# Optimization experiments

Hardware: AMD Instinct MI355X
Metric: run time of the kernel (lower is better)

Reference implementation:

```python
import jax, jax.numpy as jnp
import numpy as np

T, B, V, E, H = 128, 32, 32000, 512, 1024
PAD = 0

def setup_inputs() -> dict:
    key = jax.random.key(0)
    ks = jax.random.split(key, 10)
    indices = jax.random.randint(ks[0], (T, B), 0, V)
    emb = jax.random.normal(ks[1], (V, E), jnp.float32) * 0.02
    s = 1.0 / np.sqrt(H).astype(np.float32)
    W_ih = jax.random.normal(ks[2], (4 * H, E), jnp.float32) * s
    W_hh = jax.random.normal(ks[3], (4 * H, H), jnp.float32) * s
    b_ih = jax.random.normal(ks[4], (4 * H,), jnp.float32) * 0.01
    b_hh = jax.random.normal(ks[5], (4 * H,), jnp.float32) * 0.01
    W_out = jax.random.normal(ks[6], (V, H), jnp.float32) * s
    b_out = jnp.zeros((V,), jnp.float32)
    h0 = jax.random.uniform(ks[7], (B, H), jnp.float32, -0.1, 0.1)
    c0 = jax.random.uniform(ks[8], (B, H), jnp.float32, -0.1, 0.1)
    return dict(indices=indices, emb=emb, W_ih=W_ih, W_hh=W_hh,
                b_ih=b_ih, b_hh=b_hh, W_out=W_out, b_out=b_out, h0=h0, c0=c0)

def reference(indices, emb, W_ih, W_hh, b_ih, b_hh, W_out, b_out, h0, c0):
    # embed + relu for all timesteps at once (dropout_rate=0.0 -> identity)
    x_all = jax.nn.relu(emb[indices[:-1]])   # [T-1, B, E]
    targets = indices[1:]                    # [T-1, B]

    def step(carry, inp):
        h, c, loss = carry
        x, tgt = inp
        # torch LSTM gate order: i, f, g, o
        gates = x @ W_ih.T + b_ih + h @ W_hh.T + b_hh   # [B, 4H]
        i, f, g, o = jnp.split(gates, 4, axis=-1)
        c = jax.nn.sigmoid(f) * c + jax.nn.sigmoid(i) * jnp.tanh(g)
        h = jax.nn.sigmoid(o) * jnp.tanh(c)
        logp = jax.nn.log_softmax(h @ W_out.T + b_out, axis=-1)  # [B, V]
        nll = -jnp.take_along_axis(logp, tgt[:, None], axis=-1)[:, 0]
        # NLLLoss(reduction='sum', ignore_index=PAD)
        loss = loss + jnp.sum(jnp.where(tgt != PAD, nll, 0.0))
        return (h, c, loss), None

    (_, _, loss), _ = jax.lax.scan(step, (h0, c0, jnp.float32(0.0)), (x_all, targets))
    return loss
```

## Files before the change

### kernel.cpp

```cpp
#include <hip/hip_runtime.h>
#include <hip/hip_bf16.h>
#include <hip/hip_cooperative_groups.h>
#include <math.h>

namespace cg = cooperative_groups;

typedef __bf16 bf16_t;
typedef bf16_t bf16x8 __attribute__((ext_vector_type(8)));
typedef float f32x4 __attribute__((ext_vector_type(4)));

#define T_SEQ 128
#define NB 32
#define NV 32000
#define NE 512
#define NH 1024
#define G4 4096
#define MROWS 4064
#define MPAD 4096

#define NBLK 256

__device__ __forceinline__ void g2lds16(const bf16_t* g, bf16_t* l) {
  __builtin_amdgcn_global_load_lds((const __attribute__((address_space(1))) void*)g,
                                   (__attribute__((address_space(3))) void*)l, 16, 0, 0);
}

__device__ __forceinline__ unsigned short bf16bits(float x) {
  bf16_t b = (bf16_t)x;
  return __builtin_bit_cast(unsigned short, b);
}

__global__ void k_prep(const int* __restrict__ idx, const float* __restrict__ emb,
                       const float* __restrict__ W_ih, const float* __restrict__ W_hh,
                       const float* __restrict__ b_ih, const float* __restrict__ b_hh,
                       const float* __restrict__ W_out, const float* __restrict__ h0,
                       bf16_t* __restrict__ W_ih_bf, bf16_t* __restrict__ W_hh_bf,
                       bf16_t* __restrict__ W_out_bf, bf16_t* __restrict__ x_bf,
                       bf16_t* __restrict__ h_all, bf16_t* __restrict__ h0_bf,
                       float* __restrict__ bc, float* __restrict__ rowS,
                       int* __restrict__ tgt, unsigned* __restrict__ bar) {
  const long nW_ih = 4096L * 512;
  const long nW_hh = 4096L * 1024;
  const long nW_out = 32000L * 1024;
  const long nX = 4096L * 512;
  const long nH0 = 32L * 1024;
  const long nHpad = 32L * 1024;
  const long NTOTAL = nW_ih + nW_hh + nW_out + nX + nH0 + nHpad + 3 * 4096L + 1024;
  long stride = (long)gridDim.x * blockDim.x;
  for (long i = (long)blockIdx.x * blockDim.x + threadIdx.x; i < NTOTAL; i += stride) {
    long j = i;
    if (j < nW_ih) { W_ih_bf[j] = (bf16_t)W_ih[j]; continue; }
    j -= nW_ih;
    if (j < nW_hh) { W_hh_bf[j] = (bf16_t)W_hh[j]; continue; }
    j -= nW_hh;
    if (j < nW_out) { W_out_bf[j] = (bf16_t)W_out[j]; continue; }
    j -= nW_out;
    if (j < nX) {
      long m = j >> 9; int e = (int)(j & 511);
      float x = 0.f;
      if (m < MROWS) { x = emb[(long)idx[m] * NE + e]; x = x > 0.f ? x : 0.f; }
      x_bf[j] = (bf16_t)x; continue;
    }
    j -= nX;
    if (j < nH0) { h0_bf[j] = (bf16_t)h0[j]; continue; }
    j -= nH0;
    if (j < nHpad) { h_all[4161536L + j] = (bf16_t)0.f; continue; }
    j -= nHpad;
    if (j < 4096) { bc[j] = b_ih[j] + b_hh[j]; continue; }
    j -= 4096;
    if (j < 4096) { rowS[j] = 0.f; continue; }
    j -= 4096;
    if (j < 4096) { tgt[j] = (j < MROWS) ? idx[j + NB] : 0; continue; }
    j -= 4096;
    { bar[j] = 0u; continue; }
  }
}

__global__ __launch_bounds__(256) void k_gemm1(const bf16_t* __restrict__ A,
                                               const bf16_t* __restrict__ B,
                                               const float* __restrict__ bc,
                                               bf16_t* __restrict__ C) {
  const int K = 512;
  int tid = threadIdx.x, wid = tid >> 6, lane = tid & 63;
  int wm = wid & 1, wn = wid >> 1;
  int quad = lane >> 4, l15 = lane & 15;
  int mBase = blockIdx.x * 64, nBase = blockIdx.y * 128;

  const bf16x8* pa0 = (const bf16x8*)(A + (long)(mBase + wm * 32 + l15) * K + quad * 8);
  const bf16x8* pa1 = (const bf16x8*)(A + (long)(mBase + wm * 32 + 16 + l15) * K + quad * 8);
  const bf16x8* pb[4];
#pragma unroll
  for (int j = 0; j < 4; ++j)
    pb[j] = (const bf16x8*)(B + (long)(nBase + wn * 64 + j * 16 + l15) * K + quad * 8);

  f32x4 acc[2][4];
#pragma unroll
  for (int mi = 0; mi < 2; ++mi)
#pragma unroll
    for (int ni = 0; ni < 4; ++ni) acc[mi][ni] = (f32x4){0.f, 0.f, 0.f, 0.f};

  for (int kk = 0; kk < K / 32; ++kk) {
    bf16x8 a0 = pa0[kk * 4], a1 = pa1[kk * 4];
    bf16x8 b0 = pb[0][kk * 4], b1 = pb[1][kk * 4], b2 = pb[2][kk * 4], b3 = pb[3][kk * 4];
    acc[0][0] = __builtin_amdgcn_mfma_f32_16x16x32_bf16(a0, b0, acc[0][0], 0, 0, 0);
    acc[0][1] = __builtin_amdgcn_mfma_f32_16x16x32_bf16(a0, b1, acc[0][1], 0, 0, 0);
    acc[0][2] = __builtin_amdgcn_mfma_f32_16x16x32_bf16(a0, b2, acc[0][2], 0, 0, 0);
    acc[0][3] = __builtin_amdgcn_mfma_f32_16x16x32_bf16(a0, b3, acc[0][3], 0, 0, 0);
    acc[1][0] = __builtin_amdgcn_mfma_f32_16x16x32_bf16(a1, b0, acc[1][0], 0, 0, 0);
    acc[1][1] = __builtin_amdgcn_mfma_f32_16x16x32_bf16(a1, b1, acc[1][1], 0, 0, 0);
    acc[1][2] = __builtin_amdgcn_mfma_f32_16x16x32_bf16(a1, b2, acc[1][2], 0, 0, 0);
    acc[1][3] = __builtin_amdgcn_mfma_f32_16x16x32_bf16(a1, b3, acc[1][3], 0, 0, 0);
  }
#pragma unroll
  for (int ni = 0; ni < 4; ++ni) {
    int col = nBase + wn * 64 + ni * 16 + l15;
    float bcv = bc[col];
#pragma unroll
    for (int mi = 0; mi < 2; ++mi)
#pragma unroll
      for (int r = 0; r < 4; ++r) {
        int row = mBase + wm * 32 + mi * 16 + quad * 4 + r;
        C[(long)row * G4 + col] = (bf16_t)(acc[mi][ni][r] + bcv);
      }
  }
}

__device__ __forceinline__ void lbar(unsigned* grp, unsigned* root, unsigned* gen,
                                     unsigned target) {
  __syncthreads();
  if (threadIdx.x == 0) {
    asm volatile("" ::: "memory");
    __builtin_amdgcn_s_waitcnt(0x0f70);
    unsigned o = __hip_atomic_fetch_add(grp, 1u, __ATOMIC_RELAXED,
                                        __HIP_MEMORY_SCOPE_AGENT);
    if ((o & 15u) == 15u) {
      unsigned r = __hip_atomic_fetch_add(root, 1u, __ATOMIC_RELAXED,
                                          __HIP_MEMORY_SCOPE_AGENT);
      if ((r & 7u) == 7u)
        __hip_atomic_store(gen, (r >> 3) + 1u, __ATOMIC_RELAXED,
                           __HIP_MEMORY_SCOPE_AGENT);
    }
    while (__hip_atomic_load(gen, __ATOMIC_RELAXED, __HIP_MEMORY_SCOPE_AGENT) < target)
      __builtin_amdgcn_s_sleep(1);
    asm volatile("" ::: "memory");
  }
  __syncthreads();
}

__global__ __launch_bounds__(512) void k_rec4(const bf16_t* __restrict__ gates_x,
                                              const bf16_t* __restrict__ W_hh_bf,
                                              const bf16_t* __restrict__ h0_bf,
                                              bf16_t* __restrict__ h_all,
                                              const float* __restrict__ c0,
                                              unsigned* __restrict__ bar) {
  __shared__ float red[2 * 16 * 16 * 4];

  int bid = blockIdx.x;
  int mi = bid & 1;
  int hb = bid >> 1;
  int gbase = hb * 8;
  int tid = threadIdx.x, wid = tid >> 6, lane = tid & 63;
  int cg = wid & 1, kh = wid >> 1;
  int quad = lane >> 4, l15 = lane & 15;

  int wrow = (cg ? 2048 : 0) + ((l15 & 8) ? 1024 : 0) + gbase + (l15 & 7);
  const bf16x8* pw = (const bf16x8*)(W_hh_bf + (long)wrow * NH + kh * 256 + quad * 8);
  bf16x8 wfrag[8];
#pragma unroll
  for (int kk = 0; kk < 8; ++kk) wfrag[kk] = pw[kk * 4];

  unsigned* grp = bar + mi * 512 + (hb & 7) * 32;
  unsigned* root = bar + mi * 512 + 256;
  unsigned* gen = bar + mi * 512 + 288;

  int pb = tid >> 2, pu2 = (tid & 3) * 2;
  int u0 = gbase + pu2;
  int bglob = mi * 16 + pb;
  float cst0 = 0.f, cst1 = 0.f;
  if (tid < 64) {
    cst0 = c0[(long)bglob * NH + u0];
    cst1 = c0[(long)bglob * NH + u0 + 1];
  }
  unsigned* h32 = (unsigned*)h_all;

  for (int t = 0; t < T_SEQ - 1; ++t) {
    unsigned gxi2 = 0, gxf2 = 0, gxg2 = 0, gxo2 = 0;
    if (tid < 64) {
      const unsigned* gp = (const unsigned*)(gates_x + (long)(t * NB + bglob) * G4);
      int q = u0 >> 1;
      gxi2 = gp[q]; gxf2 = gp[512 + q]; gxg2 = gp[1024 + q]; gxo2 = gp[1536 + q];
    }

    const bf16_t* hp = (t == 0) ? h0_bf : (h_all + (long)(t - 1) * NB * NH);
    const bf16x8* pa = (const bf16x8*)(hp + (long)(mi * 16 + l15) * NH + kh * 256 + quad * 8);
    f32x4 acc = (f32x4){0.f, 0.f, 0.f, 0.f};
#pragma unroll
    for (int kk = 0; kk < 8; ++kk) {
      bf16x8 a = pa[kk * 4];
      acc = __builtin_amdgcn_mfma_f32_16x16x32_bf16(a, wfrag[kk], acc, 0, 0, 0);
    }
#pragma unroll
    for (int r = 0; r < 4; ++r) {
      int b = quad * 4 + r;
      red[(((cg << 4) + b) << 6) + (l15 << 2) + kh] = acc[r];
    }
    __syncthreads();

    if (tid < 64) {
      const float4* rp = (const float4*)red;
      float hv[2];
#pragma unroll
      for (int d = 0; d < 2; ++d) {
        int q = pu2 + d;
        float4 vi = rp[(pb << 4) + q];
        float4 vf = rp[(pb << 4) + 8 + q];
        float4 vg = rp[((16 + pb) << 4) + q];
        float4 vo = rp[((16 + pb) << 4) + 8 + q];
        unsigned bi = d ? (gxi2 & 0xffff0000u) : (gxi2 << 16);
        unsigned bff = d ? (gxf2 & 0xffff0000u) : (gxf2 << 16);
        unsigned bg = d ? (gxg2 & 0xffff0000u) : (gxg2 << 16);
        unsigned bo = d ? (gxo2 & 0xffff0000u) : (gxo2 << 16);
        float iv = vi.x + vi.y + vi.z + vi.w + __builtin_bit_cast(float, bi);
        float fv = vf.x + vf.y + vf.z + vf.w + __builtin_bit_cast(float, bff);
        float gv = vg.x + vg.y + vg.z + vg.w + __builtin_bit_cast(float, bg);
        float ov = vo.x + vo.y + vo.z + vo.w + __builtin_bit_cast(float, bo);
        float si = 1.f / (1.f + __expf(-iv));
        float sf = 1.f / (1.f + __expf(-fv));
        float so = 1.f / (1.f + __expf(-ov));
        float tg = 1.f - 2.f / (__expf(2.f * gv) + 1.f);
        float& cs = d ? cst1 : cst0;
        cs = sf * cs + si * tg;
        float th = 1.f - 2.f / (__expf(2.f * cs) + 1.f);
        hv[d] = so * th;
      }
      unsigned pack = (unsigned)bf16bits(hv[0]) | ((unsigned)bf16bits(hv[1]) << 16);
      __hip_atomic_store(&h32[(long)(t * NB + bglob) * 512 + (u0 >> 1)], pack,
                         __ATOMIC_RELAXED, __HIP_MEMORY_SCOPE_AGENT);
    }
    if (t < T_SEQ - 2) lbar(grp, root, gen, (unsigned)(t + 1));
  }
}

__global__ __launch_bounds__(256) void k_gemm2(const bf16_t* __restrict__ A,
                                               const bf16_t* __restrict__ B,
                                               const float* __restrict__ b_out,
                                               float* __restrict__ rowS) {
  __shared__ bf16_t As[128 * 32];
  __shared__ bf16_t Bs[128 * 32];
  const int K = 1024;
  int tid = threadIdx.x, wid = tid >> 6, lane = tid & 63;
  int wm = wid & 1, wn = wid >> 1;
  int quad = lane >> 4, l15 = lane & 15;
  int mBase = blockIdx.x * 128, nBase = blockIdx.y * 128;

  int rc = lane >> 2, seg = lane & 3;
  int cA0 = 2 * wid, cA1 = 2 * wid + 1;
  const bf16_t* gA0 = A + (size_t)(mBase + cA0 * 16 + rc) * K + seg * 8;
  const bf16_t* gA1 = A + (size_t)(mBase + cA1 * 16 + rc) * K + seg * 8;
  const bf16_t* gB0 = B + (size_t)(nBase + cA0 * 16 + rc) * K + seg * 8;
  const bf16_t* gB1 = B + (size_t)(nBase + cA1 * 16 + rc) * K + seg * 8;
  bf16_t* lA0 = As + cA0 * 512;
  bf16_t* lA1 = As + cA1 * 512;
  bf16_t* lB0 = Bs + cA0 * 512;
  bf16_t* lB1 = Bs + cA1 * 512;

  const bf16x8* pa[4];
  const bf16x8* pbf[4];
#pragma unroll
  for (int i = 0; i < 4; ++i) {
    pa[i] = (const bf16x8*)(As + (wm * 64 + i * 16 + l15) * 32 + quad * 8);
    pbf[i] = (const bf16x8*)(Bs + (wn * 64 + i * 16 + l15) * 32 + quad * 8);
  }

  f32x4 acc[4][4];
#pragma unroll
  for (int i = 0; i < 4; ++i)
#pragma unroll
    for (int j = 0; j < 4; ++j) acc[i][j] = (f32x4){0.f, 0.f, 0.f, 0.f};

  for (int kt = 0; kt < K / 32; ++kt) {
    g2lds16(gA0 + kt * 32, lA0);
    g2lds16(gA1 + kt * 32, lA1);
    g2lds16(gB0 + kt * 32, lB0);
    g2lds16(gB1 + kt * 32, lB1);
    __syncthreads();

    bf16x8 af[4], bf[4];
#pragma unroll
    for (int i = 0; i < 4; ++i) { af[i] = *pa[i]; bf[i] = *pbf[i]; }
#pragma unroll
    for (int i = 0; i < 4; ++i)
#pragma unroll
      for (int j = 0; j < 4; ++j)
        acc[i][j] = __builtin_amdgcn_mfma_f32_16x16x32_bf16(af[i], bf[j], acc[i][j], 0, 0, 0);
    __syncthreads();
  }

#pragma unroll
  for (int i = 0; i < 4; ++i) {
    float rs[4] = {0.f, 0.f, 0.f, 0.f};
#pragma unroll
    for (int j = 0; j < 4; ++j) {
      int col = nBase + wn * 64 + j * 16 + l15;
      float bb = b_out[col];
#pragma unroll
      for (int r = 0; r < 4; ++r) rs[r] += __expf(acc[i][j][r] + bb);
    }
#pragma unroll
    for (int r = 0; r < 4; ++r) {
#pragma unroll
      for (int s = 1; s < 16; s <<= 1) rs[r] += __shfl_xor(rs[r], s);
      if (l15 == 0) {
        int row = mBase + wm * 64 + i * 16 + quad * 4 + r;
        if (row < MROWS) atomicAdd(&rowS[row], rs[r]);
      }
    }
  }
}

__global__ __launch_bounds__(256) void k_tgt(const bf16_t* __restrict__ h_all,
                                             const bf16_t* __restrict__ W_out_bf,
                                             const float* __restrict__ b_out,
                                             const int* __restrict__ tgt,
                                             float* __restrict__ tgt_logit) {
  int gw = (int)((blockIdx.x * blockDim.x + threadIdx.x) >> 6);
  int lane = threadIdx.x & 63;
  if (gw >= MROWS) return;
  int v = tgt[gw];
  const bf16x8* ph = (const bf16x8*)(h_all + (long)gw * NH + lane * 16);
  const bf16x8* pw = (const bf16x8*)(W_out_bf + (long)v * NH + lane * 16);
  float acc = 0.f;
#pragma unroll
  for (int j = 0; j < 2; ++j) {
    bf16x8 h8 = ph[j], w8 = pw[j];
#pragma unroll
    for (int q = 0; q < 8; ++q) acc += (float)h8[q] * (float)w8[q];
  }
#pragma unroll
  for (int s = 1; s < 64; s <<= 1) acc += __shfl_xor(acc, s);
  if (lane == 0) tgt_logit[gw] = acc + b_out[v];
}

__global__ __launch_bounds__(256) void k_loss(const float* __restrict__ rowS,
                                              const float* __restrict__ tl,
                                              const int* __restrict__ tgt,
                                              float* __restrict__ out) {
  __shared__ float sm[256];
  float s = 0.f;
  for (int i = threadIdx.x; i < MROWS; i += 256)
    if (tgt[i] != 0) s += logf(rowS[i]) - tl[i];
  sm[threadIdx.x] = s;
  __syncthreads();
  for (int off = 128; off > 0; off >>= 1) {
    if (threadIdx.x < off) sm[threadIdx.x] += sm[threadIdx.x + off];
    __syncthreads();
  }
  if (threadIdx.x == 0) out[0] = sm[0];
}

extern "C" void kernel_launch(void* const* d_in, const int* in_sizes, int n_in,
                              void* d_out, int out_size, void* d_ws, size_t ws_size,
                              hipStream_t stream) {
  const int* idx = (const int*)d_in[0];
  const float* emb = (const float*)d_in[1];
  const float* W_ih = (const float*)d_in[2];
  const float* W_hh = (const float*)d_in[3];
  const float* b_ih = (const float*)d_in[4];
  const float* b_hh = (const float*)d_in[5];
  const float* W_out = (const float*)d_in[6];
  const float* b_out = (const float*)d_in[7];
  const float* h0 = (const float*)d_in[8];
  const float* c0 = (const float*)d_in[9];

  char* ws = (char*)d_ws;
  bf16_t* W_ih_bf = (bf16_t*)ws;            ws += 4096L * 512 * 2;
  bf16_t* W_hh_bf = (bf16_t*)ws;            ws += 4096L * 1024 * 2;
  bf16_t* W_out_bf = (bf16_t*)ws;           ws += 32000L * 1024 * 2;
  bf16_t* x_bf = (bf16_t*)ws;               ws += 4096L * 512 * 2;
  bf16_t* gates_x = (bf16_t*)ws;            ws += 4096L * 4096 * 2;
  bf16_t* h_all = (bf16_t*)ws;              ws += 4096L * 1024 * 2;
  bf16_t* h0_bf = (bf16_t*)ws;              ws += 32L * 1024 * 2;
  float* bc = (float*)ws;                   ws += 4096L * 4;
  float* rowS = (float*)ws;                 ws += 4096L * 4;
  float* tgt_logit = (float*)ws;            ws += 4096L * 4;
  int* tgt = (int*)ws;                      ws += 4096L * 4;
  unsigned* bar = (unsigned*)ws;            ws += 1024L * 4;

  k_prep<<<4096, 256, 0, stream>>>(idx, emb, W_ih, W_hh, b_ih, b_hh, W_out, h0,
                                   W_ih_bf, W_hh_bf, W_out_bf, x_bf, h_all, h0_bf,
                                   bc, rowS, tgt, bar);

  k_gemm1<<<dim3(64, 32), 256, 0, stream>>>(x_bf, W_ih_bf, bc, gates_x);

  {
    void* args[] = {(void*)&gates_x, (void*)&W_hh_bf, (void*)&h0_bf, (void*)&h_all,
                    (void*)&c0, (void*)&bar};
    hipLaunchCooperativeKernel((void*)k_rec4, dim3(NBLK), dim3(512), args, 0, stream);
  }

  k_gemm2<<<dim3(32, 250), 256, 0, stream>>>(h_all, W_out_bf, b_out, rowS);

  k_tgt<<<1016, 256, 0, stream>>>(h_all, W_out_bf, b_out, tgt, tgt_logit);

  k_loss<<<1, 256, 0, stream>>>(rowS, tgt_logit, tgt, (float*)d_out);
}
```

Measured before the change: 1.330 ms.

## Replace hierarchical atomic grid barrier with per-block step flags in LSTM recurrence

The two-level atomic counter barrier between timesteps is replaced by per-block progress slots. Each block publishes the step it has finished; wave 0 polls all 128 slots of its batch half with a ballot, then releases the block's other waves through an LDS flag. This removes the serialized atomic chain and the extra block-wide syncs on the critical path of every timestep. In exchange, every block polls 128 global words per step and the other waves spin on shared memory.

```diff
diff --git a/kernel.cpp b/kernel.cpp
--- a/kernel.cpp
+++ b/kernel.cpp
@@ -17,8 +17,6 @@
 #define G4 4096
 #define MROWS 4064
 #define MPAD 4096
-
-#define NBLK 256
 
 __device__ __forceinline__ void g2lds16(const bf16_t* g, bf16_t* l) {
   __builtin_amdgcn_global_load_lds((const __attribute__((address_space(1))) void*)g,
@@ -125,35 +123,14 @@
   }
 }
 
-__device__ __forceinline__ void lbar(unsigned* grp, unsigned* root, unsigned* gen,
-                                     unsigned target) {
-  __syncthreads();
-  if (threadIdx.x == 0) {
-    asm volatile("" ::: "memory");
-    __builtin_amdgcn_s_waitcnt(0x0f70);
-    unsigned o = __hip_atomic_fetch_add(grp, 1u, __ATOMIC_RELAXED,
-                                        __HIP_MEMORY_SCOPE_AGENT);
-    if ((o & 15u) == 15u) {
-      unsigned r = __hip_atomic_fetch_add(root, 1u, __ATOMIC_RELAXED,
-                                          __HIP_MEMORY_SCOPE_AGENT);
-      if ((r & 7u) == 7u)
-        __hip_atomic_store(gen, (r >> 3) + 1u, __ATOMIC_RELAXED,
-                           __HIP_MEMORY_SCOPE_AGENT);
-    }
-    while (__hip_atomic_load(gen, __ATOMIC_RELAXED, __HIP_MEMORY_SCOPE_AGENT) < target)
-      __builtin_amdgcn_s_sleep(1);
-    asm volatile("" ::: "memory");
-  }
-  __syncthreads();
-}
-
-__global__ __launch_bounds__(512) void k_rec4(const bf16_t* __restrict__ gates_x,
+__global__ __launch_bounds__(512) void k_rec6(const bf16_t* __restrict__ gates_x,
                                               const bf16_t* __restrict__ W_hh_bf,
                                               const bf16_t* __restrict__ h0_bf,
                                               bf16_t* __restrict__ h_all,
                                               const float* __restrict__ c0,
                                               unsigned* __restrict__ bar) {
   __shared__ float red[2 * 16 * 16 * 4];
+  __shared__ unsigned go;
 
   int bid = blockIdx.x;
   int mi = bid & 1;
@@ -169,9 +146,7 @@
 #pragma unroll
   for (int kk = 0; kk < 8; ++kk) wfrag[kk] = pw[kk * 4];
 
-  unsigned* grp = bar + mi * 512 + (hb & 7) * 32;
-  unsigned* root = bar + mi * 512 + 256;
-  unsigned* gen = bar + mi * 512 + 288;
+  unsigned* slots = bar + mi * 128;
 
   int pb = tid >> 2, pu2 = (tid & 3) * 2;
   int u0 = gbase + pu2;
@@ -183,12 +158,34 @@
   }
   unsigned* h32 = (unsigned*)h_all;
 
+  if (tid == 0) go = 0;
+  __syncthreads();
+
   for (int t = 0; t < T_SEQ - 1; ++t) {
     unsigned gxi2 = 0, gxf2 = 0, gxg2 = 0, gxo2 = 0;
-    if (tid < 64) {
+    if (wid == 0) {
       const unsigned* gp = (const unsigned*)(gates_x + (long)(t * NB + bglob) * G4);
       int q = u0 >> 1;
       gxi2 = gp[q]; gxf2 = gp[512 + q]; gxg2 = gp[1024 + q]; gxo2 = gp[1536 + q];
+    }
+
+    if (t > 0) {
+      unsigned tv = (unsigned)t;
+      if (wid == 0) {
+        for (;;) {
+          unsigned s0 = __hip_atomic_load(&slots[lane], __ATOMIC_RELAXED,
+                                          __HIP_MEMORY_SCOPE_AGENT);
+          unsigned s1 = __hip_atomic_load(&slots[64 + lane], __ATOMIC_RELAXED,
+                                          __HIP_MEMORY_SCOPE_AGENT);
+          if (__ballot((s0 >= tv) && (s1 >= tv)) == ~0ull) break;
+          __builtin_amdgcn_s_sleep(1);
+        }
+        if (lane == 0)
+          __hip_atomic_store(&go, tv, __ATOMIC_RELAXED, __HIP_MEMORY_SCOPE_WORKGROUP);
+      } else {
+        while (__hip_atomic_load(&go, __ATOMIC_RELAXED, __HIP_MEMORY_SCOPE_WORKGROUP) < tv)
+          __builtin_amdgcn_s_sleep(1);
+      }
     }
 
     const bf16_t* hp = (t == 0) ? h0_bf : (h_all + (long)(t - 1) * NB * NH);
@@ -237,7 +234,13 @@
       __hip_atomic_store(&h32[(long)(t * NB + bglob) * 512 + (u0 >> 1)], pack,
                          __ATOMIC_RELAXED, __HIP_MEMORY_SCOPE_AGENT);
     }
-    if (t < T_SEQ - 2) lbar(grp, root, gen, (unsigned)(t + 1));
+
+    if (t < T_SEQ - 2 && wid == 0) {
+      __builtin_amdgcn_s_waitcnt(0x0f70);
+      if (lane == 0)
+        __hip_atomic_store(&slots[hb], (unsigned)(t + 1), __ATOMIC_RELAXED,
+                           __HIP_MEMORY_SCOPE_AGENT);
+    }
   }
 }
 
@@ -395,7 +398,7 @@
   {
     void* args[] = {(void*)&gates_x, (void*)&W_hh_bf, (void*)&h0_bf, (void*)&h_all,
                     (void*)&c0, (void*)&bar};
-    hipLaunchCooperativeKernel((void*)k_rec4, dim3(NBLK), dim3(512), args, 0, stream);
+    hipLaunchCooperativeKernel((void*)k_rec6, dim3(256), dim3(512), args, 0, stream);
   }
 
   k_gemm2<<<dim3(32, 250), 256, 0, stream>>>(h_all, W_out_bf, b_out, rowS);
```

Result: slower. 1.455 ms (+9.4%).
